# Performance work log

Measured on AMD Instinct MI355X. Metric: run time of the kernel, lower is better.

## Reference

```python
import jax, jax.numpy as jnp
import numpy as np

B, A, D = 256, 32, 2048  # batch, num attributes, hidden_dim


def setup_inputs() -> dict:
    key = jax.random.key(0)
    k1, k2, k3, k4, k5 = jax.random.split(key, 5)
    x = jax.random.normal(k1, (B, D), dtype=jnp.float32)
    attribute_feat = jax.random.normal(k2, (B, A, D), dtype=jnp.float32)
    attribute_label = jax.random.randint(k3, (B, A), 0, 2, dtype=jnp.int64)
    # GraphConvolution parameters (glorot-style scale)
    W = jax.random.normal(k4, (D, D), dtype=jnp.float32) * (1.0 / np.sqrt(D))
    b = jnp.zeros((D,), dtype=jnp.float32)
    return {"x": x, "attribute_feat": attribute_feat,
            "attribute_label": attribute_label, "W": W, "b": b}


def reference(x, attribute_feat, attribute_label, W, b):
    # Star adjacency: nonzero attribute nodes <-> global node (index A)
    mask = (attribute_label > 0).astype(x.dtype)            # [B, A]
    adj = jnp.zeros((B, A + 1, A + 1), dtype=x.dtype)
    adj = adj.at[:, :A, A].set(mask).at[:, A, :A].set(mask)  # [B, A+1, A+1]
    # Vertex features: attributes + global node (x) per sample
    vertex = jnp.concatenate([attribute_feat, x[:, None, :]], axis=1)  # [B, A+1, D]
    # GCN layer: tanh(adj @ (vertex @ W) + b); dropout is identity in eval
    support = jnp.einsum('bnd,de->bne', vertex, W)           # [B, A+1, D]
    out = jnp.tanh(jnp.einsum('bnm,bmd->bnd', adj, support) + b)
    # Return updated global-node embedding per sample
    return out[:, -1, :]                                     # [B, D]
```

## Files before the change

### kernel.cpp

```cpp
#include <hip/hip_runtime.h>
#include <hip/hip_bf16.h>

typedef unsigned short ushort_t;
using ushort4v = __attribute__((ext_vector_type(4))) ushort_t;
using ushort8 = __attribute__((ext_vector_type(8))) ushort_t;
using short8  = __attribute__((ext_vector_type(8))) short;
using float4v = __attribute__((ext_vector_type(4))) float;

#define Bsz 256
#define Aattr 32
#define Ddim 2048

__device__ __forceinline__ float bf2f(ushort_t u) {
    union { unsigned int i; float f; } c;
    c.i = ((unsigned int)u) << 16;
    return c.f;
}

__device__ __forceinline__ ushort_t f2bf(float f) {
    union { float f; unsigned int i; } c;
    c.f = f;
    unsigned int x = c.i;
    unsigned int r = (x + 0x7FFFu + ((x >> 16) & 1u)) >> 16;
    return (ushort_t)r;
}

struct BfPair { ushort_t hi, lo; };
__device__ __forceinline__ BfPair split_bf16(float x) {
    BfPair p;
    p.hi = f2bf(x);
    p.lo = f2bf(x - bf2f(p.hi));
    return p;
}

__global__ __launch_bounds__(256) void k_prep(
    const float* __restrict__ feat, const int* __restrict__ label,
    const float* __restrict__ W,
    ushort_t* __restrict__ s_hi, ushort_t* __restrict__ s_lo,
    ushort_t* __restrict__ WT_hi, ushort_t* __restrict__ WT_lo) {
    __shared__ float tile[64][65];
    const int t = threadIdx.x;

    if (blockIdx.x < 512) {
        int* list = (int*)&tile[0][0];
        int* cntp = (int*)&tile[1][0];
        const int b    = blockIdx.x >> 1;
        const int half = blockIdx.x & 1;

        if (t < 64) {
            int lab = label[b * Aattr + (t & 31)];
            unsigned long long vote = __ballot(lab > 0);
            unsigned m32 = (unsigned)(vote & 0xFFFFFFFFull);
            if (t < 32) {
                if (lab > 0) {
                    int rank = __popc(m32 & ((1u << t) - 1u));
                    list[rank] = t;
                }
                if (t == 0) *cntp = __popc(m32);
            }
        }
        __syncthreads();

        const int n  = *cntp;
        const int d0 = half * 1024 + t * 4;
        const float* fb = feat + (size_t)b * (Aattr * Ddim) + d0;

        float a0 = 0.f, a1 = 0.f, a2 = 0.f, a3 = 0.f;
        int i = 0;
        for (; i + 4 <= n; i += 4) {
            const int j0 = list[i], j1 = list[i+1], j2 = list[i+2], j3 = list[i+3];
            float4 v0 = *(const float4*)(fb + j0 * Ddim);
            float4 v1 = *(const float4*)(fb + j1 * Ddim);
            float4 v2 = *(const float4*)(fb + j2 * Ddim);
            float4 v3 = *(const float4*)(fb + j3 * Ddim);
            a0 += v0.x + v1.x + v2.x + v3.x;
            a1 += v0.y + v1.y + v2.y + v3.y;
            a2 += v0.z + v1.z + v2.z + v3.z;
            a3 += v0.w + v1.w + v2.w + v3.w;
        }
        for (; i < n; ++i) {
            float4 v = *(const float4*)(fb + list[i] * Ddim);
            a0 += v.x; a1 += v.y; a2 += v.z; a3 += v.w;
        }

        ushort4v hi, lo;
        BfPair p0 = split_bf16(a0); hi[0] = p0.hi; lo[0] = p0.lo;
        BfPair p1 = split_bf16(a1); hi[1] = p1.hi; lo[1] = p1.lo;
        BfPair p2 = split_bf16(a2); hi[2] = p2.hi; lo[2] = p2.lo;
        BfPair p3 = split_bf16(a3); hi[3] = p3.hi; lo[3] = p3.lo;
        *(ushort4v*)(s_hi + (size_t)b * Ddim + d0) = hi;
        *(ushort4v*)(s_lo + (size_t)b * Ddim + d0) = lo;
    } else {
        const int q  = blockIdx.x - 512;
        const int bx = q & 31;
        const int by = q >> 5;

#pragma unroll
        for (int p = 0; p < 4; ++p) {
            const int row = p * 16 + (t >> 4);
            const int c   = (t & 15) * 4;
            float4 v = *(const float4*)(W + (size_t)(by * 64 + row) * Ddim + bx * 64 + c);
            tile[row][c + 0] = v.x;
            tile[row][c + 1] = v.y;
            tile[row][c + 2] = v.z;
            tile[row][c + 3] = v.w;
        }
        __syncthreads();
#pragma unroll
        for (int p = 0; p < 2; ++p) {
            const int er = p * 32 + (t >> 3);
            const int dc = (t & 7) * 8;
            ushort8 hi, lo;
#pragma unroll
            for (int j = 0; j < 8; ++j) {
                BfPair pr = split_bf16(tile[dc + j][er]);
                hi[j] = pr.hi; lo[j] = pr.lo;
            }
            const size_t off = (size_t)(bx * 64 + er) * Ddim + by * 64 + dc;
            *(ushort8*)(WT_hi + off) = hi;
            *(ushort8*)(WT_lo + off) = lo;
        }
    }
}

__global__ __launch_bounds__(512) void k_gemm2(
    const ushort_t* __restrict__ S_hi, const ushort_t* __restrict__ S_lo,
    const ushort_t* __restrict__ WT_hi, const ushort_t* __restrict__ WT_lo,
    const float* __restrict__ bias, float* __restrict__ out) {
    __shared__ float red[8][32 * 68];

    const int g      = blockIdx.x;
    const int q      = g >> 3;
    const int n_tile = (g & 7) * 4 + (q & 3);
    const int m_tile = q >> 2;
    const int m0     = m_tile * 64;
    const int n0     = n_tile * 64;

    const int t    = threadIdx.x;
    const int w    = t >> 6;
    const int wm   = w >> 2;
    const int wk   = w & 3;
    const int l    = t & 63;
    const int quad = l >> 4;
    const int m16  = l & 15;
    const int k0   = wk * 512;

    float4v acc[2][4];
#pragma unroll
    for (int i = 0; i < 2; ++i)
#pragma unroll
        for (int j = 0; j < 4; ++j) acc[i][j] = {0.f, 0.f, 0.f, 0.f};

    const size_t aoff = (size_t)(m0 + wm * 32 + m16) * Ddim + quad * 8;
    const size_t boff = (size_t)(n0 + m16) * Ddim + quad * 8;
    const ushort_t* Ah = S_hi + aoff;
    const ushort_t* Al = S_lo + aoff;
    const ushort_t* Bh = WT_hi + boff;
    const ushort_t* Bl = WT_lo + boff;

    for (int k = k0; k < k0 + 512; k += 32) {
        short8 ah0 = *(const short8*)(Ah + k);
        short8 ah1 = *(const short8*)(Ah + 16 * Ddim + k);
        short8 al0 = *(const short8*)(Al + k);
        short8 al1 = *(const short8*)(Al + 16 * Ddim + k);
        short8 bh[4], bl[4];
#pragma unroll
        for (int i = 0; i < 4; ++i) {
            const size_t o = (size_t)(i * 16) * Ddim + k;
            bh[i] = *(const short8*)(Bh + o);
            bl[i] = *(const short8*)(Bl + o);
        }
#pragma unroll
        for (int ni = 0; ni < 4; ++ni) {
            acc[0][ni] = __builtin_amdgcn_mfma_f32_16x16x32_bf16(ah0, bh[ni], acc[0][ni], 0, 0, 0);
            acc[0][ni] = __builtin_amdgcn_mfma_f32_16x16x32_bf16(ah0, bl[ni], acc[0][ni], 0, 0, 0);
            acc[0][ni] = __builtin_amdgcn_mfma_f32_16x16x32_bf16(al0, bh[ni], acc[0][ni], 0, 0, 0);
            acc[1][ni] = __builtin_amdgcn_mfma_f32_16x16x32_bf16(ah1, bh[ni], acc[1][ni], 0, 0, 0);
            acc[1][ni] = __builtin_amdgcn_mfma_f32_16x16x32_bf16(ah1, bl[ni], acc[1][ni], 0, 0, 0);
            acc[1][ni] = __builtin_amdgcn_mfma_f32_16x16x32_bf16(al1, bh[ni], acc[1][ni], 0, 0, 0);
        }
    }

#pragma unroll
    for (int mi = 0; mi < 2; ++mi) {
#pragma unroll
        for (int ni = 0; ni < 4; ++ni) {
#pragma unroll
            for (int rr = 0; rr < 4; ++rr) {
                red[w][(mi * 16 + quad * 4 + rr) * 68 + ni * 16 + m16] = acc[mi][ni][rr];
            }
        }
    }
    __syncthreads();

    const int m_l  = t >> 3;
    const int n_l  = (t & 7) * 8;
    const int half = m_l >> 5;
    const int base = (m_l & 31) * 68 + n_l;
    float s[8];
#pragma unroll
    for (int j = 0; j < 8; ++j) s[j] = 0.f;
#pragma unroll
    for (int ww = 0; ww < 4; ++ww) {
        float4 v0 = *(const float4*)&red[half * 4 + ww][base];
        float4 v1 = *(const float4*)&red[half * 4 + ww][base + 4];
        s[0] += v0.x; s[1] += v0.y; s[2] += v0.z; s[3] += v0.w;
        s[4] += v1.x; s[5] += v1.y; s[6] += v1.z; s[7] += v1.w;
    }
    float4 b0 = *(const float4*)(bias + n0 + n_l);
    float4 b1 = *(const float4*)(bias + n0 + n_l + 4);
    float4 o0, o1;
    o0.x = tanhf(s[0] + b0.x);
    o0.y = tanhf(s[1] + b0.y);
    o0.z = tanhf(s[2] + b0.z);
    o0.w = tanhf(s[3] + b0.w);
    o1.x = tanhf(s[4] + b1.x);
    o1.y = tanhf(s[5] + b1.y);
    o1.z = tanhf(s[6] + b1.z);
    o1.w = tanhf(s[7] + b1.w);
    float* op = out + (size_t)(m0 + m_l) * Ddim + n0 + n_l;
    *(float4*)op = o0;
    *(float4*)(op + 4) = o1;
}

extern "C" void kernel_launch(void* const* d_in, const int* in_sizes, int n_in,
                              void* d_out, int out_size, void* d_ws, size_t ws_size,
                              hipStream_t stream) {
    const float* feat  = (const float*)d_in[1];
    const int*   label = (const int*)d_in[2];
    const float* W     = (const float*)d_in[3];
    const float* bias  = (const float*)d_in[4];
    float*       out   = (float*)d_out;

    char* ws = (char*)d_ws;
    ushort_t* s_hi  = (ushort_t*)ws;
    ushort_t* s_lo  = (ushort_t*)(ws + (1u << 20));
    ushort_t* WT_hi = (ushort_t*)(ws + (2u << 20));
    ushort_t* WT_lo = (ushort_t*)(ws + (10u << 20));

    k_prep<<<dim3(1536), dim3(256), 0, stream>>>(feat, label, W, s_hi, s_lo, WT_hi, WT_lo);
    k_gemm2<<<dim3(128), dim3(512), 0, stream>>>(s_hi, s_lo, WT_hi, WT_lo, bias, out);
}
```

Measured before the change: 155.8 us.

## Tile bf16 operands into MFMA-friendly blocks and split GEMM into more blocks

The prep kernel now writes the split-bf16 activation sums and transposed weights in a 16x32 tiled layout, so each MFMA fragment load reads one contiguous 1KB tile. The GEMM kernel halves the M tile to 32 rows, doubling the grid to 256 blocks, and gives each of the 8 waves a 256-wide K slice, reduced through shared memory. It also double-buffers the fragment registers and adds an occupancy hint of 2 blocks per CU. The aim is better memory coalescing and more parallelism, at the cost of re-reading weight tiles across twice as many M tiles and higher register pressure.

```diff
diff --git a/kernel.cpp b/kernel.cpp
--- a/kernel.cpp
+++ b/kernel.cpp
@@ -10,6 +10,9 @@
 #define Bsz 256
 #define Aattr 32
 #define Ddim 2048
+
+#define KT (Ddim / 32)
+#define ROWTILE (KT * 512)
 
 __device__ __forceinline__ float bf2f(ushort_t u) {
     union { unsigned int i; float f; } c;
@@ -31,6 +34,10 @@
     p.hi = f2bf(x);
     p.lo = f2bf(x - bf2f(p.hi));
     return p;
+}
+
+__device__ __forceinline__ size_t tiled_off(int row, int k) {
+    return (size_t)((row >> 4) * KT + (k >> 5)) * 512 + (row & 15) * 32 + (k & 31);
 }
 
 __global__ __launch_bounds__(256) void k_prep(
@@ -88,8 +95,9 @@
         BfPair p1 = split_bf16(a1); hi[1] = p1.hi; lo[1] = p1.lo;
         BfPair p2 = split_bf16(a2); hi[2] = p2.hi; lo[2] = p2.lo;
         BfPair p3 = split_bf16(a3); hi[3] = p3.hi; lo[3] = p3.lo;
-        *(ushort4v*)(s_hi + (size_t)b * Ddim + d0) = hi;
-        *(ushort4v*)(s_lo + (size_t)b * Ddim + d0) = lo;
+        const size_t off = tiled_off(b, d0);
+        *(ushort4v*)(s_hi + off) = hi;
+        *(ushort4v*)(s_lo + off) = lo;
     } else {
         const int q  = blockIdx.x - 512;
         const int bx = q & 31;
@@ -116,14 +124,14 @@
                 BfPair pr = split_bf16(tile[dc + j][er]);
                 hi[j] = pr.hi; lo[j] = pr.lo;
             }
-            const size_t off = (size_t)(bx * 64 + er) * Ddim + by * 64 + dc;
+            const size_t off = tiled_off(bx * 64 + er, by * 64 + dc);
             *(ushort8*)(WT_hi + off) = hi;
             *(ushort8*)(WT_lo + off) = lo;
         }
     }
 }
 
-__global__ __launch_bounds__(512) void k_gemm2(
+__global__ __launch_bounds__(512, 2) void k_gemm2(
     const ushort_t* __restrict__ S_hi, const ushort_t* __restrict__ S_lo,
     const ushort_t* __restrict__ WT_hi, const ushort_t* __restrict__ WT_lo,
     const float* __restrict__ bias, float* __restrict__ out) {
@@ -133,17 +141,14 @@
     const int q      = g >> 3;
     const int n_tile = (g & 7) * 4 + (q & 3);
     const int m_tile = q >> 2;
-    const int m0     = m_tile * 64;
+    const int m0     = m_tile * 32;
     const int n0     = n_tile * 64;
 
     const int t    = threadIdx.x;
     const int w    = t >> 6;
-    const int wm   = w >> 2;
-    const int wk   = w & 3;
     const int l    = t & 63;
     const int quad = l >> 4;
     const int m16  = l & 15;
-    const int k0   = wk * 512;
 
     float4v acc[2][4];
 #pragma unroll
@@ -151,35 +156,45 @@
 #pragma unroll
         for (int j = 0; j < 4; ++j) acc[i][j] = {0.f, 0.f, 0.f, 0.f};
 
-    const size_t aoff = (size_t)(m0 + wm * 32 + m16) * Ddim + quad * 8;
-    const size_t boff = (size_t)(n0 + m16) * Ddim + quad * 8;
-    const ushort_t* Ah = S_hi + aoff;
-    const ushort_t* Al = S_lo + aoff;
-    const ushort_t* Bh = WT_hi + boff;
-    const ushort_t* Bl = WT_lo + boff;
-
-    for (int k = k0; k < k0 + 512; k += 32) {
-        short8 ah0 = *(const short8*)(Ah + k);
-        short8 ah1 = *(const short8*)(Ah + 16 * Ddim + k);
-        short8 al0 = *(const short8*)(Al + k);
-        short8 al1 = *(const short8*)(Al + 16 * Ddim + k);
-        short8 bh[4], bl[4];
-#pragma unroll
-        for (int i = 0; i < 4; ++i) {
-            const size_t o = (size_t)(i * 16) * Ddim + k;
-            bh[i] = *(const short8*)(Bh + o);
-            bl[i] = *(const short8*)(Bl + o);
-        }
+    const int lane_off = m16 * 32 + quad * 8;
+    const size_t abase = (size_t)((m0 >> 4) * KT + w * 8) * 512 + lane_off;
+    const size_t bbase = (size_t)((n0 >> 4) * KT + w * 8) * 512 + lane_off;
+    const ushort_t* pAh = S_hi + abase;
+    const ushort_t* pAl = S_lo + abase;
+    const ushort_t* pBh = WT_hi + bbase;
+    const ushort_t* pBl = WT_lo + bbase;
+
+    short8 Ah_[2][2], Al_[2][2], Bh_[2][4], Bl_[2][4];
+
+#define LOADSET(buf, it)                                                     \
+    do {                                                                     \
+        Ah_[buf][0] = *(const short8*)(pAh + (it) * 512);                    \
+        Ah_[buf][1] = *(const short8*)(pAh + ROWTILE + (it) * 512);          \
+        Al_[buf][0] = *(const short8*)(pAl + (it) * 512);                    \
+        Al_[buf][1] = *(const short8*)(pAl + ROWTILE + (it) * 512);          \
+        _Pragma("unroll")                                                    \
+        for (int i_ = 0; i_ < 4; ++i_) {                                     \
+            Bh_[buf][i_] = *(const short8*)(pBh + i_ * ROWTILE + (it) * 512);\
+            Bl_[buf][i_] = *(const short8*)(pBl + i_ * ROWTILE + (it) * 512);\
+        }                                                                    \
+    } while (0)
+
+    LOADSET(0, 0);
+#pragma unroll
+    for (int it = 0; it < 8; ++it) {
+        const int cur = it & 1;
+        if (it < 7) LOADSET(cur ^ 1, it + 1);
 #pragma unroll
         for (int ni = 0; ni < 4; ++ni) {
-            acc[0][ni] = __builtin_amdgcn_mfma_f32_16x16x32_bf16(ah0, bh[ni], acc[0][ni], 0, 0, 0);
-            acc[0][ni] = __builtin_amdgcn_mfma_f32_16x16x32_bf16(ah0, bl[ni], acc[0][ni], 0, 0, 0);
-            acc[0][ni] = __builtin_amdgcn_mfma_f32_16x16x32_bf16(al0, bh[ni], acc[0][ni], 0, 0, 0);
-            acc[1][ni] = __builtin_amdgcn_mfma_f32_16x16x32_bf16(ah1, bh[ni], acc[1][ni], 0, 0, 0);
-            acc[1][ni] = __builtin_amdgcn_mfma_f32_16x16x32_bf16(ah1, bl[ni], acc[1][ni], 0, 0, 0);
-            acc[1][ni] = __builtin_amdgcn_mfma_f32_16x16x32_bf16(al1, bh[ni], acc[1][ni], 0, 0, 0);
-        }
-    }
+            acc[0][ni] = __builtin_amdgcn_mfma_f32_16x16x32_bf16(Ah_[cur][0], Bh_[cur][ni], acc[0][ni], 0, 0, 0);
+            acc[0][ni] = __builtin_amdgcn_mfma_f32_16x16x32_bf16(Ah_[cur][0], Bl_[cur][ni], acc[0][ni], 0, 0, 0);
+            acc[0][ni] = __builtin_amdgcn_mfma_f32_16x16x32_bf16(Al_[cur][0], Bh_[cur][ni], acc[0][ni], 0, 0, 0);
+            acc[1][ni] = __builtin_amdgcn_mfma_f32_16x16x32_bf16(Ah_[cur][1], Bh_[cur][ni], acc[1][ni], 0, 0, 0);
+            acc[1][ni] = __builtin_amdgcn_mfma_f32_16x16x32_bf16(Ah_[cur][1], Bl_[cur][ni], acc[1][ni], 0, 0, 0);
+            acc[1][ni] = __builtin_amdgcn_mfma_f32_16x16x32_bf16(Al_[cur][1], Bh_[cur][ni], acc[1][ni], 0, 0, 0);
+        }
+    }
+#undef LOADSET
 
 #pragma unroll
     for (int mi = 0; mi < 2; ++mi) {
@@ -193,34 +208,22 @@
     }
     __syncthreads();
 
-    const int m_l  = t >> 3;
-    const int n_l  = (t & 7) * 8;
-    const int half = m_l >> 5;
-    const int base = (m_l & 31) * 68 + n_l;
-    float s[8];
-#pragma unroll
-    for (int j = 0; j < 8; ++j) s[j] = 0.f;
-#pragma unroll
-    for (int ww = 0; ww < 4; ++ww) {
-        float4 v0 = *(const float4*)&red[half * 4 + ww][base];
-        float4 v1 = *(const float4*)&red[half * 4 + ww][base + 4];
-        s[0] += v0.x; s[1] += v0.y; s[2] += v0.z; s[3] += v0.w;
-        s[4] += v1.x; s[5] += v1.y; s[6] += v1.z; s[7] += v1.w;
+    const int m_l  = t >> 4;
+    const int n_l  = (t & 15) * 4;
+    const int base = m_l * 68 + n_l;
+    float s0 = 0.f, s1 = 0.f, s2 = 0.f, s3 = 0.f;
+#pragma unroll
+    for (int ww = 0; ww < 8; ++ww) {
+        float4 v = *(const float4*)&red[ww][base];
+        s0 += v.x; s1 += v.y; s2 += v.z; s3 += v.w;
     }
     float4 b0 = *(const float4*)(bias + n0 + n_l);
-    float4 b1 = *(const float4*)(bias + n0 + n_l + 4);
-    float4 o0, o1;
-    o0.x = tanhf(s[0] + b0.x);
-    o0.y = tanhf(s[1] + b0.y);
-    o0.z = tanhf(s[2] + b0.z);
-    o0.w = tanhf(s[3] + b0.w);
-    o1.x = tanhf(s[4] + b1.x);
-    o1.y = tanhf(s[5] + b1.y);
-    o1.z = tanhf(s[6] + b1.z);
-    o1.w = tanhf(s[7] + b1.w);
-    float* op = out + (size_t)(m0 + m_l) * Ddim + n0 + n_l;
-    *(float4*)op = o0;
-    *(float4*)(op + 4) = o1;
+    float4 o0;
+    o0.x = tanhf(s0 + b0.x);
+    o0.y = tanhf(s1 + b0.y);
+    o0.z = tanhf(s2 + b0.z);
+    o0.w = tanhf(s3 + b0.w);
+    *(float4*)(out + (size_t)(m0 + m_l) * Ddim + n0 + n_l) = o0;
 }
 
 extern "C" void kernel_launch(void* const* d_in, const int* in_sizes, int n_in,
@@ -239,5 +242,5 @@
     ushort_t* WT_lo = (ushort_t*)(ws + (10u << 20));
 
     k_prep<<<dim3(1536), dim3(256), 0, stream>>>(feat, label, W, s_hi, s_lo, WT_hi, WT_lo);
-    k_gemm2<<<dim3(128), dim3(512), 0, stream>>>(s_hi, s_lo, WT_hi, WT_lo, bias, out);
-}
+    k_gemm2<<<dim3(256), dim3(512), 0, stream>>>(s_hi, s_lo, WT_hi, WT_lo, bias, out);
+}
```

After: 128.5 us. -17.5%, faster.
